# Performance work log

Hardware: AMD Instinct MI355X
Metric: run time of the kernel (lower is better)

## Reference

```python
import jax, jax.numpy as jnp
import numpy as np

EMA_OLD = 0.01  # original: m[z] = m[z]*0.01 + y*0.99
EMA_NEW = 0.99

def setup_inputs() -> dict:
    key = jax.random.key(0)
    k1, k2, k3, k4 = jax.random.split(key, 4)
    B, n, C, L = 4096, 1024, 64, 64
    y = jax.random.normal(k1, (B, C, L), dtype=jnp.float32)   # encoder latents
    m = jax.random.normal(k2, (n, C, L), dtype=jnp.float32)   # codebook means
    sd = jax.random.uniform(k3, (n, C, L), dtype=jnp.float32) # codebook variances (init ones in orig)
    p = jax.random.uniform(k4, (n,), dtype=jnp.float32)       # cluster counts
    return {"y": y, "m": m, "sd": sd, "p": p}

def reference(y, m, sd, p):
    B, C, L = y.shape
    n = m.shape[0]
    # pairwise squared distances via ||y||^2 - 2 y.m + ||m||^2 (GEMM form)
    yf = y.reshape(B, C * L)
    mf = m.reshape(n, C * L)
    d2 = ((yf * yf).sum(-1, keepdims=True)
          - 2.0 * (yf @ mf.T)
          + (mf * mf).sum(-1)[None, :])            # [B, n]
    z = jnp.argmin(d2, axis=1)                      # [B] assignments
    new_m = m.at[z].set(m[z] * EMA_OLD + y * EMA_NEW)
    # original updates sd using the ALREADY-updated m gathered at z
    mg = new_m[z]
    new_sd = sd.at[z].set((mg - y) ** 2 * EMA_OLD + sd[z] * EMA_NEW)
    return jnp.concatenate([new_m, new_sd], axis=0)  # [2n, C, L]
```

## Files before the change

kernel.cpp:

```cpp
#include <hip/hip_runtime.h>

#define B_ROWS 4096
#define N_CLUST 1024
#define KDIM 4096
#define NKT 32

#define EMA_OLD 0.01f
#define EMA_NEW 0.99f
#define MARGIN 2.0f

typedef unsigned short ushortT;
typedef _Float16 half8 __attribute__((ext_vector_type(8)));
typedef float f32x16 __attribute__((ext_vector_type(16)));

#define WS_WINNER_OFF 0
#define WS_Z_OFF      4096
#define WS_YY_OFF     20480
#define WS_MM_OFF     36864
#define WS_D2_OFF     65536
#define WS_YHI_OFF    (WS_D2_OFF + 16777216)
#define WS_MHI_OFF    (WS_YHI_OFF + 33554432)
#define WS_END        (WS_MHI_OFF + 8388608)

__global__ __launch_bounds__(256) void convert_sumsq(
    const float* __restrict__ ysrc, const float* __restrict__ msrc,
    ushortT* __restrict__ yhi, ushortT* __restrict__ mhi,
    float* __restrict__ yy, float* __restrict__ mm) {
    const int blk = blockIdx.x;
    const float* src;
    ushortT* hi;
    float* out;
    int row;
    if (blk < B_ROWS) {
        src = ysrc; hi = yhi; out = yy + blk; row = blk;
    } else {
        row = blk - B_ROWS;
        src = msrc; hi = mhi; out = mm + row;
    }
    const int r = row & 63, rb = row >> 6;
    const int t = threadIdx.x;
    float s = 0.f;
#pragma unroll
    for (int h = 0; h < 2; ++h) {
        int ci = h * 256 + t;
        int kt = ci >> 4, p = ci & 15;
        int c = p ^ (r & 15);
        const float* sp = src + ((size_t)row << 12) + kt * 128 + c * 8;
        float4 v0 = *(const float4*)sp;
        float4 v1 = *(const float4*)(sp + 4);
        float vv[8] = {v0.x, v0.y, v0.z, v0.w, v1.x, v1.y, v1.z, v1.w};
        half8 hv;
#pragma unroll
        for (int i = 0; i < 8; ++i) {
            hv[i] = (_Float16)vv[i];
            s += vv[i] * vv[i];
        }
        size_t off = (((size_t)rb * NKT + kt) * 64 + r) * 128 + p * 8;
        *(half8*)(hi + off) = hv;
    }
    for (int off = 32; off > 0; off >>= 1) s += __shfl_down(s, off, 64);
    __shared__ float red[4];
    if ((t & 63) == 0) red[t >> 6] = s;
    __syncthreads();
    if (t == 0) out[0] = red[0] + red[1] + red[2] + red[3];
}

__device__ __forceinline__ void gload_lds16(const void* g, void* l) {
    __builtin_amdgcn_global_load_lds(
        (const __attribute__((address_space(1))) unsigned int*)g,
        (__attribute__((address_space(3))) unsigned int*)l, 16, 0, 0);
}

__device__ __forceinline__ half8 ldfrag(const ushortT* s, int r, int c) {
    int p = c ^ (r & 15);
    return *(const half8*)(s + r * 128 + p * 8);
}

__global__ __launch_bounds__(256, 4) void screen_gemm(
    const ushortT* __restrict__ Ah, const ushortT* __restrict__ Bh,
    const float* __restrict__ yy, const float* __restrict__ mm,
    float* __restrict__ d2ws) {
    __shared__ __align__(16) ushortT sA[64 * 128];
    __shared__ __align__(16) ushortT sB[64 * 128];

    const int t = threadIdx.x, w = t >> 6, l = t & 63;
    const int bx = blockIdx.x >> 4, by = blockIdx.x & 15;
    const int row0 = bx * 64, col0 = by * 64;
    const int wr = (w >> 1) * 32, wc = (w & 1) * 32;
    const int m0 = l & 31, hsel = l >> 5;

    const char* gA = (const char*)Ah + (size_t)bx * (NKT * 16384) + l * 16;
    const char* gB = (const char*)Bh + (size_t)by * (NKT * 16384) + l * 16;

    f32x16 acc;
#pragma unroll
    for (int i = 0; i < 16; ++i) acc[i] = 0.f;

    for (int kt = 0; kt < NKT; ++kt) {
        __syncthreads();
#pragma unroll
        for (int j = 0; j < 4; ++j) {
            int ch = w * 4 + j;
            gload_lds16(gA + (size_t)kt * 16384 + ch * 1024, (char*)sA + ch * 1024);
            gload_lds16(gB + (size_t)kt * 16384 + ch * 1024, (char*)sB + ch * 1024);
        }
        __syncthreads();
#pragma unroll
        for (int kk = 0; kk < 8; ++kk) {
            int c = kk * 2 + hsel;
            half8 ah = ldfrag(sA, wr + m0, c);
            half8 bh = ldfrag(sB, wc + m0, c);
            acc = __builtin_amdgcn_mfma_f32_32x32x16_f16(ah, bh, acc, 0, 0, 0);
        }
    }

    const int gcol = col0 + wc + m0;
    const float mv = mm[gcol];
#pragma unroll
    for (int r = 0; r < 16; ++r) {
        int ri = (r & 3) + 8 * (r >> 2) + 4 * hsel;
        int grow = row0 + wr + ri;
        d2ws[(size_t)grow * N_CLUST + gcol] = yy[grow] - 2.0f * acc[r] + mv;
    }
}

__global__ __launch_bounds__(256) void rescreen(
    const float* __restrict__ d2ws, const float* __restrict__ ysrc,
    const float* __restrict__ msrc, const float* __restrict__ yy,
    const float* __restrict__ mm, int* __restrict__ z) {
    const int row = blockIdx.x * 4 + (threadIdx.x >> 6);
    const int l = threadIdx.x & 63;
    const float* dr = d2ws + (size_t)row * N_CLUST;

    float v[16];
#pragma unroll
    for (int k = 0; k < 16; ++k) v[k] = dr[l + 64 * k];

    float mn = v[0];
#pragma unroll
    for (int k = 1; k < 16; ++k) mn = fminf(mn, v[k]);
#pragma unroll
    for (int s = 1; s <= 32; s <<= 1) mn = fminf(mn, __shfl_xor(mn, s, 64));
    const float thr = mn + MARGIN;

    int cnt = 0;
#pragma unroll
    for (int k = 0; k < 16; ++k) cnt += (v[k] <= thr) ? 1 : 0;
#pragma unroll
    for (int s = 1; s <= 32; s <<= 1) cnt += __shfl_xor(cnt, s, 64);

    int zj;
    if (cnt == 1) {
        int cj = 0x7FFFFFFF;
#pragma unroll
        for (int k = 0; k < 16; ++k)
            if (v[k] <= thr) cj = min(cj, l + 64 * k);
#pragma unroll
        for (int s = 1; s <= 32; s <<= 1) cj = min(cj, __shfl_xor(cj, s, 64));
        zj = cj;
    } else {
        double bestd = 1e300;
        int bestj = -1;
        const float4* yp = (const float4*)(ysrc + (size_t)row * KDIM);
        for (int k = 0; k < 16; ++k) {
            unsigned long long mask = __ballot(v[k] <= thr);
            while (mask) {
                int lb = __ffsll((unsigned long long)mask) - 1;
                mask &= mask - 1;
                int j = 64 * k + lb;
                const float4* mp = (const float4*)(msrc + (size_t)j * KDIM);
                double acc = 0.0;
#pragma unroll
                for (int tt = 0; tt < 16; ++tt) {
                    float4 a = yp[l + 64 * tt];
                    float4 b = mp[l + 64 * tt];
                    acc += (double)a.x * b.x + (double)a.y * b.y +
                           (double)a.z * b.z + (double)a.w * b.w;
                }
#pragma unroll
                for (int s = 1; s <= 32; s <<= 1)
                    acc += __shfl_xor(acc, s, 64);
                double d2x = (double)yy[row] - 2.0 * acc + (double)mm[j];
                if (d2x < bestd) { bestd = d2x; bestj = j; }
            }
        }
        zj = bestj;
    }
    if (l == 0) z[row] = zj;
}

__global__ void pick_winner(const int* __restrict__ z,
                            int* __restrict__ winner) {
    int b = blockIdx.x * blockDim.x + threadIdx.x;
    if (b < B_ROWS) atomicMax(&winner[z[b]], b);
}

__global__ __launch_bounds__(256) void write_out(
    const float* __restrict__ y, const float* __restrict__ m,
    const float* __restrict__ sd, const int* __restrict__ winner,
    float* __restrict__ out) {
    const int idx = blockIdx.x;
    const int t = threadIdx.x;
    const int w = winner[idx];
    const float4* mp = (const float4*)(m + (size_t)idx * KDIM);
    const float4* sp = (const float4*)(sd + (size_t)idx * KDIM);
    float4* om = (float4*)(out + (size_t)idx * KDIM);
    float4* os = (float4*)(out + (size_t)(N_CLUST + idx) * KDIM);
    if (w >= 0) {
        const float4* yp = (const float4*)(y + (size_t)w * KDIM);
        for (int i = t; i < KDIM / 4; i += 256) {
            float4 mv = mp[i], yv = yp[i], sv = sp[i];
            float4 nm, ns;
            nm.x = mv.x * EMA_OLD + yv.x * EMA_NEW;
            nm.y = mv.y * EMA_OLD + yv.y * EMA_NEW;
            nm.z = mv.z * EMA_OLD + yv.z * EMA_NEW;
            nm.w = mv.w * EMA_OLD + yv.w * EMA_NEW;
            float dx = nm.x - yv.x, dy = nm.y - yv.y;
            float dz = nm.z - yv.z, dw = nm.w - yv.w;
            ns.x = dx * dx * EMA_OLD + sv.x * EMA_NEW;
            ns.y = dy * dy * EMA_OLD + sv.y * EMA_NEW;
            ns.z = dz * dz * EMA_OLD + sv.z * EMA_NEW;
            ns.w = dw * dw * EMA_OLD + sv.w * EMA_NEW;
            om[i] = nm;
            os[i] = ns;
        }
    } else {
        for (int i = t; i < KDIM / 4; i += 256) {
            om[i] = mp[i];
            os[i] = sp[i];
        }
    }
}

extern "C" void kernel_launch(void* const* d_in, const int* in_sizes, int n_in,
                              void* d_out, int out_size, void* d_ws,
                              size_t ws_size, hipStream_t stream) {
    const float* y  = (const float*)d_in[0];
    const float* m  = (const float*)d_in[1];
    const float* sd = (const float*)d_in[2];
    float* out = (float*)d_out;

    char* ws = (char*)d_ws;
    int* winner = (int*)(ws + WS_WINNER_OFF);
    int* z      = (int*)(ws + WS_Z_OFF);
    float* yy   = (float*)(ws + WS_YY_OFF);
    float* mm   = (float*)(ws + WS_MM_OFF);
    float* d2ws = (float*)(ws + WS_D2_OFF);
    ushortT* yhi = (ushortT*)(ws + WS_YHI_OFF);
    ushortT* mhi = (ushortT*)(ws + WS_MHI_OFF);

    hipMemsetAsync(winner, 0xFF, 4096, stream);

    convert_sumsq<<<B_ROWS + N_CLUST, 256, 0, stream>>>(y, m, yhi, mhi, yy, mm);

    screen_gemm<<<(B_ROWS / 64) * (N_CLUST / 64), 256, 0, stream>>>(
        yhi, mhi, yy, mm, d2ws);

    rescreen<<<B_ROWS / 4, 256, 0, stream>>>(d2ws, y, m, yy, mm, z);

    pick_winner<<<B_ROWS / 256, 256, 0, stream>>>(z, winner);
    write_out<<<N_CLUST, 256, 0, stream>>>(y, m, sd, winner, out);
}
```

Measured before the change: 226.6 us.

## Enlarge screen GEMM tiles to 128x128 and double-buffer LDS loads

The screening GEMM block tile grows from 64x64 to 128x128, and each wave now computes a 2x2 set of 32x32 MFMA accumulators instead of one. This reuses each loaded fragment across more MFMAs and halves the global traffic per output. Global-to-LDS loads are double-buffered: the next k-tile is staged while the current one is computed, using an explicit vmcnt wait. The cost is 128KB of LDS and launch bounds of 1 block per CU, and the grid shrinks to 256 blocks, which may underfill a 256-CU device.

Result: no change. 229.7 us (+1.4%).

```diff
diff --git a/kernel.cpp b/kernel.cpp
--- a/kernel.cpp
+++ b/kernel.cpp
@@ -76,52 +76,92 @@
     return *(const half8*)(s + r * 128 + p * 8);
 }
 
-__global__ __launch_bounds__(256, 4) void screen_gemm(
+__global__ __launch_bounds__(256, 1) void screen_gemm(
     const ushortT* __restrict__ Ah, const ushortT* __restrict__ Bh,
     const float* __restrict__ yy, const float* __restrict__ mm,
     float* __restrict__ d2ws) {
-    __shared__ __align__(16) ushortT sA[64 * 128];
-    __shared__ __align__(16) ushortT sB[64 * 128];
+    __shared__ __align__(16) ushortT sA[2][2 * 64 * 128];
+    __shared__ __align__(16) ushortT sB[2][2 * 64 * 128];
 
     const int t = threadIdx.x, w = t >> 6, l = t & 63;
-    const int bx = blockIdx.x >> 4, by = blockIdx.x & 15;
-    const int row0 = bx * 64, col0 = by * 64;
-    const int wr = (w >> 1) * 32, wc = (w & 1) * 32;
+    const int bx = blockIdx.x >> 3, by = blockIdx.x & 7;
+    const int row0 = bx * 128, col0 = by * 128;
+    const int wr = (w >> 1) * 64, wc = (w & 1) * 64;
     const int m0 = l & 31, hsel = l >> 5;
 
-    const char* gA = (const char*)Ah + (size_t)bx * (NKT * 16384) + l * 16;
-    const char* gB = (const char*)Bh + (size_t)by * (NKT * 16384) + l * 16;
-
-    f32x16 acc;
-#pragma unroll
-    for (int i = 0; i < 16; ++i) acc[i] = 0.f;
+    const char* gAbase = (const char*)Ah + (size_t)l * 16;
+    const char* gBbase = (const char*)Bh + (size_t)l * 16;
+
+    f32x16 acc[2][2];
+#pragma unroll
+    for (int i = 0; i < 2; ++i)
+#pragma unroll
+        for (int j = 0; j < 2; ++j)
+#pragma unroll
+            for (int r = 0; r < 16; ++r) acc[i][j][r] = 0.f;
+
+#define STAGE(buf, kt)                                                        \
+    {                                                                         \
+        _Pragma("unroll")                                                     \
+        for (int j = 0; j < 8; ++j) {                                         \
+            int ch = w * 8 + j;                                               \
+            int tile = ch >> 4, seg = ch & 15;                                \
+            size_t go = ((size_t)((2 * bx + tile) * NKT + (kt)) << 14) +      \
+                        seg * 1024;                                           \
+            gload_lds16(gAbase + go,                                          \
+                        (char*)&sA[buf][0] + tile * 16384 + seg * 1024);      \
+            size_t gob = ((size_t)((2 * by + tile) * NKT + (kt)) << 14) +     \
+                         seg * 1024;                                          \
+            gload_lds16(gBbase + gob,                                         \
+                        (char*)&sB[buf][0] + tile * 16384 + seg * 1024);      \
+        }                                                                     \
+    }
+
+    STAGE(0, 0);
 
     for (int kt = 0; kt < NKT; ++kt) {
-        __syncthreads();
-#pragma unroll
-        for (int j = 0; j < 4; ++j) {
-            int ch = w * 4 + j;
-            gload_lds16(gA + (size_t)kt * 16384 + ch * 1024, (char*)sA + ch * 1024);
-            gload_lds16(gB + (size_t)kt * 16384 + ch * 1024, (char*)sB + ch * 1024);
-        }
-        __syncthreads();
+        const int buf = kt & 1;
+        if (kt + 1 < NKT) {
+            STAGE(buf ^ 1, kt + 1);
+            asm volatile("s_waitcnt vmcnt(16)" ::: "memory");
+        } else {
+            asm volatile("s_waitcnt vmcnt(0)" ::: "memory");
+        }
+        __builtin_amdgcn_s_barrier();
+
+        const ushortT* tA = &sA[buf][(wr >> 6) * 8192];
+        const ushortT* tB = &sB[buf][(wc >> 6) * 8192];
 #pragma unroll
         for (int kk = 0; kk < 8; ++kk) {
             int c = kk * 2 + hsel;
-            half8 ah = ldfrag(sA, wr + m0, c);
-            half8 bh = ldfrag(sB, wc + m0, c);
-            acc = __builtin_amdgcn_mfma_f32_32x32x16_f16(ah, bh, acc, 0, 0, 0);
-        }
-    }
-
-    const int gcol = col0 + wc + m0;
-    const float mv = mm[gcol];
-#pragma unroll
-    for (int r = 0; r < 16; ++r) {
-        int ri = (r & 3) + 8 * (r >> 2) + 4 * hsel;
-        int grow = row0 + wr + ri;
-        d2ws[(size_t)grow * N_CLUST + gcol] = yy[grow] - 2.0f * acc[r] + mv;
-    }
+            half8 a0 = ldfrag(tA, m0, c);
+            half8 a1 = ldfrag(tA, 32 + m0, c);
+            half8 b0 = ldfrag(tB, m0, c);
+            half8 b1 = ldfrag(tB, 32 + m0, c);
+            acc[0][0] = __builtin_amdgcn_mfma_f32_32x32x16_f16(a0, b0, acc[0][0], 0, 0, 0);
+            acc[0][1] = __builtin_amdgcn_mfma_f32_32x32x16_f16(a0, b1, acc[0][1], 0, 0, 0);
+            acc[1][0] = __builtin_amdgcn_mfma_f32_32x32x16_f16(a1, b0, acc[1][0], 0, 0, 0);
+            acc[1][1] = __builtin_amdgcn_mfma_f32_32x32x16_f16(a1, b1, acc[1][1], 0, 0, 0);
+        }
+        asm volatile("" ::: "memory");
+        __builtin_amdgcn_s_barrier();
+    }
+#undef STAGE
+
+#pragma unroll
+    for (int i = 0; i < 2; ++i)
+#pragma unroll
+        for (int j = 0; j < 2; ++j) {
+            const int gcol = col0 + wc + j * 32 + m0;
+            const float mv = mm[gcol];
+#pragma unroll
+            for (int r = 0; r < 16; ++r) {
+                int ri = (r & 3) + 8 * (r >> 2) + 4 * hsel;
+                int grow = row0 + wr + i * 32 + ri;
+                d2ws[(size_t)grow * N_CLUST + gcol] =
+                    yy[grow] - 2.0f * acc[i][j][r] + mv;
+            }
+        }
 }
 
 __global__ __launch_bounds__(256) void rescreen(
@@ -253,7 +293,7 @@
 
     convert_sumsq<<<B_ROWS + N_CLUST, 256, 0, stream>>>(y, m, yhi, mhi, yy, mm);
 
-    screen_gemm<<<(B_ROWS / 64) * (N_CLUST / 64), 256, 0, stream>>>(
+    screen_gemm<<<(B_ROWS / 128) * (N_CLUST / 128), 256, 0, stream>>>(
         yhi, mhi, yy, mm, d2ws);
 
     rescreen<<<B_ROWS / 4, 256, 0, stream>>>(d2ws, y, m, yy, mm, z);
```

## Use 128x128 split-K tiles with int16 quantized partials and fuse winner selection

Applied to the files above, without the earlier changes.

The screening GEMM moves from 64x64 tiles to 128x128 tiles with each wave computing a 2x2 block of MFMAs, and splits K four ways so the grid stays large. Each split writes quantized int16 partial dot products instead of full fp32 distances. The rescreen kernel sums the four partials and adds the norms, and it does the atomicMax winner selection itself, which removes the pick_winner launch. The aim is more operand reuse per LDS load and less distance-matrix traffic. The cost is extra quantization error (1/16 resolution, clamped), which the 2.0 margin rescreen has to absorb, plus four partial reads per element in rescreen.

Result: faster. 217.7 us (-3.9%).

```diff
diff --git a/kernel.cpp b/kernel.cpp
--- a/kernel.cpp
+++ b/kernel.cpp
@@ -4,10 +4,12 @@
 #define N_CLUST 1024
 #define KDIM 4096
 #define NKT 32
+#define NSTEP 16
 
 #define EMA_OLD 0.01f
 #define EMA_NEW 0.99f
 #define MARGIN 2.0f
+#define PSCALE 16.0f
 
 typedef unsigned short ushortT;
 typedef _Float16 half8 __attribute__((ext_vector_type(8)));
@@ -17,8 +19,8 @@
 #define WS_Z_OFF      4096
 #define WS_YY_OFF     20480
 #define WS_MM_OFF     36864
-#define WS_D2_OFF     65536
-#define WS_YHI_OFF    (WS_D2_OFF + 16777216)
+#define WS_P_OFF      65536
+#define WS_YHI_OFF    (WS_P_OFF + 33554432)
 #define WS_MHI_OFF    (WS_YHI_OFF + 33554432)
 #define WS_END        (WS_MHI_OFF + 8388608)
 
@@ -71,70 +73,115 @@
         (__attribute__((address_space(3))) unsigned int*)l, 16, 0, 0);
 }
 
-__device__ __forceinline__ half8 ldfrag(const ushortT* s, int r, int c) {
-    int p = c ^ (r & 15);
-    return *(const half8*)(s + r * 128 + p * 8);
+__device__ __forceinline__ half8 ldfrag_pair(const ushortT* s, int r, int c) {
+    int q = r >> 1;
+    int sl = ((((r & 1) << 3) | c) ^ (q & 15));
+    return *(const half8*)(s + q * 128 + sl * 8);
 }
 
 __global__ __launch_bounds__(256, 4) void screen_gemm(
     const ushortT* __restrict__ Ah, const ushortT* __restrict__ Bh,
-    const float* __restrict__ yy, const float* __restrict__ mm,
-    float* __restrict__ d2ws) {
-    __shared__ __align__(16) ushortT sA[64 * 128];
-    __shared__ __align__(16) ushortT sB[64 * 128];
+    short* __restrict__ pws) {
+    __shared__ __align__(16) ushortT sA[128 * 64];
+    __shared__ __align__(16) ushortT sB[128 * 64];
 
     const int t = threadIdx.x, w = t >> 6, l = t & 63;
-    const int bx = blockIdx.x >> 4, by = blockIdx.x & 15;
-    const int row0 = bx * 64, col0 = by * 64;
-    const int wr = (w >> 1) * 32, wc = (w & 1) * 32;
+    const int by = blockIdx.x & 7;
+    const int kh = (blockIdx.x >> 3) & 3;
+    const int bx = blockIdx.x >> 5;
+    const int row0 = bx * 128, col0 = by * 128;
+    const int wr = (w >> 1) * 64, wc = (w & 1) * 64;
     const int m0 = l & 31, hsel = l >> 5;
 
-    const char* gA = (const char*)Ah + (size_t)bx * (NKT * 16384) + l * 16;
-    const char* gB = (const char*)Bh + (size_t)by * (NKT * 16384) + l * 16;
-
-    f32x16 acc;
-#pragma unroll
-    for (int i = 0; i < 16; ++i) acc[i] = 0.f;
-
-    for (int kt = 0; kt < NKT; ++kt) {
+    int laneoff[4];
+#pragma unroll
+    for (int j = 0; j < 4; ++j) {
+        int g = w * 4 + j;
+        int q = g * 4 + (l >> 4);
+        int u = (l & 15) ^ (q & 15);
+        int rr = 2 * q + (u >> 3);
+        int R = rr & 63;
+        int hi3 = (R >> 3) & 1;
+        laneoff[j] = R * 256 + ((((hi3 << 3) | ((u & 7) ^ (R & 7)))) << 4);
+    }
+
+    f32x16 acc[2][2];
+#pragma unroll
+    for (int i = 0; i < 2; ++i)
+#pragma unroll
+        for (int j = 0; j < 2; ++j)
+#pragma unroll
+            for (int r = 0; r < 16; ++r) acc[i][j][r] = 0.f;
+
+    const int ra0 = wr + m0, ra1 = wr + 32 + m0;
+    const int rb0 = wc + m0, rb1 = wc + 32 + m0;
+
+#pragma unroll 2
+    for (int i = 0; i < NSTEP; ++i) {
+        const int kt_ = kh * (NKT / 4) + (i >> 1);
+        const int ks_ = i & 1;
         __syncthreads();
 #pragma unroll
         for (int j = 0; j < 4; ++j) {
-            int ch = w * 4 + j;
-            gload_lds16(gA + (size_t)kt * 16384 + ch * 1024, (char*)sA + ch * 1024);
-            gload_lds16(gB + (size_t)kt * 16384 + ch * 1024, (char*)sB + ch * 1024);
+            const int g = w * 4 + j;
+            const int lo = laneoff[j] ^ (ks_ << 7);
+            const size_t tbA = ((size_t)((2 * bx + (g >> 3)) * NKT + kt_) << 14);
+            const size_t tbB = ((size_t)((2 * by + (g >> 3)) * NKT + kt_) << 14);
+            gload_lds16((const char*)Ah + tbA + lo, (char*)sA + g * 1024);
+            gload_lds16((const char*)Bh + tbB + lo, (char*)sB + g * 1024);
         }
         __syncthreads();
-#pragma unroll
-        for (int kk = 0; kk < 8; ++kk) {
+
+#pragma unroll
+        for (int kk = 0; kk < 4; ++kk) {
             int c = kk * 2 + hsel;
-            half8 ah = ldfrag(sA, wr + m0, c);
-            half8 bh = ldfrag(sB, wc + m0, c);
-            acc = __builtin_amdgcn_mfma_f32_32x32x16_f16(ah, bh, acc, 0, 0, 0);
-        }
-    }
-
-    const int gcol = col0 + wc + m0;
-    const float mv = mm[gcol];
-#pragma unroll
-    for (int r = 0; r < 16; ++r) {
-        int ri = (r & 3) + 8 * (r >> 2) + 4 * hsel;
-        int grow = row0 + wr + ri;
-        d2ws[(size_t)grow * N_CLUST + gcol] = yy[grow] - 2.0f * acc[r] + mv;
-    }
+            half8 a0 = ldfrag_pair(sA, ra0, c);
+            half8 a1 = ldfrag_pair(sA, ra1, c);
+            half8 b0 = ldfrag_pair(sB, rb0, c);
+            half8 b1 = ldfrag_pair(sB, rb1, c);
+            acc[0][0] = __builtin_amdgcn_mfma_f32_32x32x16_f16(a0, b0, acc[0][0], 0, 0, 0);
+            acc[0][1] = __builtin_amdgcn_mfma_f32_32x32x16_f16(a0, b1, acc[0][1], 0, 0, 0);
+            acc[1][0] = __builtin_amdgcn_mfma_f32_32x32x16_f16(a1, b0, acc[1][0], 0, 0, 0);
+            acc[1][1] = __builtin_amdgcn_mfma_f32_32x32x16_f16(a1, b1, acc[1][1], 0, 0, 0);
+        }
+    }
+
+    short* pk = pws + (size_t)kh * (B_ROWS * (size_t)N_CLUST);
+#pragma unroll
+    for (int i = 0; i < 2; ++i)
+#pragma unroll
+        for (int j = 0; j < 2; ++j) {
+            const int gcol = col0 + wc + j * 32 + m0;
+#pragma unroll
+            for (int r = 0; r < 16; ++r) {
+                int ri = (r & 3) + 8 * (r >> 2) + 4 * hsel;
+                int grow = row0 + wr + i * 32 + ri;
+                float q = fmaxf(fminf(acc[i][j][r] * (-2.0f * PSCALE),
+                                      32767.f), -32767.f);
+                pk[(size_t)grow * N_CLUST + gcol] = (short)__float2int_rn(q);
+            }
+        }
 }
 
 __global__ __launch_bounds__(256) void rescreen(
-    const float* __restrict__ d2ws, const float* __restrict__ ysrc,
+    const short* __restrict__ pws, const float* __restrict__ ysrc,
     const float* __restrict__ msrc, const float* __restrict__ yy,
-    const float* __restrict__ mm, int* __restrict__ z) {
+    const float* __restrict__ mm, int* __restrict__ winner) {
     const int row = blockIdx.x * 4 + (threadIdx.x >> 6);
     const int l = threadIdx.x & 63;
-    const float* dr = d2ws + (size_t)row * N_CLUST;
+    const size_t rb = (size_t)row * N_CLUST;
+    const float yyr = yy[row];
 
     float v[16];
 #pragma unroll
-    for (int k = 0; k < 16; ++k) v[k] = dr[l + 64 * k];
+    for (int k = 0; k < 16; ++k) {
+        int col = l + 64 * k;
+        int s = (int)pws[rb + col];
+        s += (int)pws[rb + col + (B_ROWS * (size_t)N_CLUST)];
+        s += (int)pws[rb + col + 2 * (B_ROWS * (size_t)N_CLUST)];
+        s += (int)pws[rb + col + 3 * (B_ROWS * (size_t)N_CLUST)];
+        v[k] = yyr + mm[col] + (float)s * (1.0f / PSCALE);
+    }
 
     float mn = v[0];
 #pragma unroll
@@ -186,13 +233,7 @@
         }
         zj = bestj;
     }
-    if (l == 0) z[row] = zj;
-}
-
-__global__ void pick_winner(const int* __restrict__ z,
-                            int* __restrict__ winner) {
-    int b = blockIdx.x * blockDim.x + threadIdx.x;
-    if (b < B_ROWS) atomicMax(&winner[z[b]], b);
+    if (l == 0) atomicMax(&winner[zj], row);
 }
 
 __global__ __launch_bounds__(256) void write_out(
@@ -242,10 +283,9 @@
 
     char* ws = (char*)d_ws;
     int* winner = (int*)(ws + WS_WINNER_OFF);
-    int* z      = (int*)(ws + WS_Z_OFF);
     float* yy   = (float*)(ws + WS_YY_OFF);
     float* mm   = (float*)(ws + WS_MM_OFF);
-    float* d2ws = (float*)(ws + WS_D2_OFF);
+    short* pws  = (short*)(ws + WS_P_OFF);
     ushortT* yhi = (ushortT*)(ws + WS_YHI_OFF);
     ushortT* mhi = (ushortT*)(ws + WS_MHI_OFF);
 
@@ -253,11 +293,10 @@
 
     convert_sumsq<<<B_ROWS + N_CLUST, 256, 0, stream>>>(y, m, yhi, mhi, yy, mm);
 
-    screen_gemm<<<(B_ROWS / 64) * (N_CLUST / 64), 256, 0, stream>>>(
-        yhi, mhi, yy, mm, d2ws);
-
-    rescreen<<<B_ROWS / 4, 256, 0, stream>>>(d2ws, y, m, yy, mm, z);
-
-    pick_winner<<<B_ROWS / 256, 256, 0, stream>>>(z, winner);
+    screen_gemm<<<(B_ROWS / 128) * (N_CLUST / 128) * 4, 256, 0, stream>>>(
+        yhi, mhi, pws);
+
+    rescreen<<<B_ROWS / 4, 256, 0, stream>>>(pws, y, m, yy, mm, winner);
+
     write_out<<<N_CLUST, 256, 0, stream>>>(y, m, sd, winner, out);
 }
```
